# Kernel tuning notes

Measured on AMD Instinct MI355X. Metric: run time of the kernel, lower is better.

## Reference

```python
import jax, jax.numpy as jnp
import numpy as np
import math

B, S, HID = 1, 4096, 2048
NH, NKV, DH = 8, 1, 256
ROPE_BASE = 10000.0


def setup_inputs() -> dict:
    key = jax.random.key(0)
    ks = jax.random.split(key, 5)
    sc = 0.02
    return {
        "hidden_states": jax.random.normal(ks[0], (B, S, HID), dtype=jnp.float32),
        "position_ids": jnp.arange(S, dtype=jnp.int32)[None, :].repeat(B, axis=0),
        "wq": jax.random.normal(ks[1], (HID, NH * DH), dtype=jnp.float32) * sc,
        "wk": jax.random.normal(ks[2], (HID, NKV * DH), dtype=jnp.float32) * sc,
        "wv": jax.random.normal(ks[3], (HID, NKV * DH), dtype=jnp.float32) * sc,
        "wo": jax.random.normal(ks[4], (NH * DH, HID), dtype=jnp.float32) * sc,
    }


def _rope_cos_sin(position_ids, dtype):
    # inv_freq: [DH/2]
    inv_freq = 1.0 / (ROPE_BASE ** (jnp.arange(0, DH, 2, dtype=jnp.float32) / DH))
    # freqs: [B, S, DH/2]
    freqs = position_ids.astype(jnp.float32)[:, :, None] * inv_freq[None, None, :]
    emb = jnp.concatenate([freqs, freqs], axis=-1)  # [B, S, DH]
    return jnp.cos(emb).astype(dtype), jnp.sin(emb).astype(dtype)


def _rotate_half(x):
    x1, x2 = x[..., : DH // 2], x[..., DH // 2 :]
    return jnp.concatenate([-x2, x1], axis=-1)


def reference(hidden_states, position_ids, wq, wk, wv, wo):
    bsz, q_len, _ = hidden_states.shape
    dtype = hidden_states.dtype

    # QKV projections (bias=False)
    q = (hidden_states @ wq).reshape(bsz, q_len, NH, DH).transpose(0, 2, 1, 3)   # [B,NH,S,DH]
    k = (hidden_states @ wk).reshape(bsz, q_len, NKV, DH).transpose(0, 2, 1, 3)  # [B,NKV,S,DH]
    v = (hidden_states @ wv).reshape(bsz, q_len, NKV, DH).transpose(0, 2, 1, 3)  # [B,NKV,S,DH]

    # RoPE (unsqueeze_dim=1 -> broadcast over heads)
    cos, sin = _rope_cos_sin(position_ids, dtype)
    cos, sin = cos[:, None, :, :], sin[:, None, :, :]  # [B,1,S,DH]
    q = q * cos + _rotate_half(q) * sin
    k = k * cos + _rotate_half(k) * sin

    # GQA: k/v broadcast over the NH head dim via matmul broadcasting (repeat_kv)
    scores = jnp.matmul(q, jnp.swapaxes(k, -1, -2)) / math.sqrt(DH)  # [B,NH,S,S]

    # additive causal mask (0 on/below diagonal, -inf-ish above)
    neg = jnp.finfo(jnp.float32).min
    causal = jnp.where(
        jnp.tril(jnp.ones((q_len, q_len), dtype=bool)), 0.0, neg
    ).astype(jnp.float32)[None, None, :, :]
    scores = scores + causal

    probs = jax.nn.softmax(scores.astype(jnp.float32), axis=-1).astype(dtype)
    attn = jnp.matmul(probs, v)  # [B,NH,S,DH] (v broadcasts over NH)

    attn = attn.transpose(0, 2, 1, 3).reshape(bsz, q_len, NH * DH)
    return attn @ wo
```

## Files before the change

### kernel.cpp

```cpp
#include <hip/hip_runtime.h>
#include <hip/hip_bf16.h>

typedef __bf16 bf16;
typedef __attribute__((ext_vector_type(8))) __bf16 bf16x8;
typedef __attribute__((ext_vector_type(4))) float f32x4;

#define S_LEN  4096
#define HIDDEN 2048
#define N_HEADS 8
#define D_HEAD 256
#define QKV_N  2560
#define NEG_BIG (-1e30f)
#define MFIX 8.0f

#define OFF_WQKVT 0u
#define OFF_WOT   10485760u
#define OFF_QKV   18874368u
#define OFF_VT    39845888u
#define OFF_AOUT  41943040u
#define OFF_FLAG  58720256u
#define WS_NEED   58720320u
#define OFF_PBUF  0u
#define OFF_LBUF  8388608u

__global__ __launch_bounds__(256) void detect_dtype(const unsigned short* __restrict__ w,
                                                    int* __restrict__ flag) {
  __shared__ int bad;
  if (threadIdx.x == 0) bad = 0;
  __syncthreads();
  int local = 0;
  for (int i = threadIdx.x; i < 4096; i += 256) {
    int e = (w[i] >> 7) & 0xFF;
    if (e >= 130) local = 1;
  }
  if (local) atomicOr(&bad, 1);
  __syncthreads();
  if (threadIdx.x == 0) *flag = bad;
}

__device__ __forceinline__ bf16x8 load8(const void* p, size_t idx, bool f32) {
  if (f32) {
    const float* q = (const float*)p + idx;
    bf16x8 r;
#pragma unroll
    for (int j = 0; j < 8; ++j) r[j] = (bf16)q[j];
    return r;
  }
  return *(const bf16x8*)((const bf16*)p + idx);
}

__global__ __launch_bounds__(256) void cvt_hs(const void* __restrict__ hs,
                                              bf16* __restrict__ dst,
                                              const int* __restrict__ flag) {
  bool f32 = (*flag != 0);
  size_t i = ((size_t)blockIdx.x * 256 + threadIdx.x) * 8;
  *(bf16x8*)(dst + i) = load8(hs, i, f32);
}

__device__ __forceinline__ void transpose_tile64(const void* __restrict__ src, size_t sbase,
                                                 int sld, bool f32,
                                                 bf16* __restrict__ dst, int dld,
                                                 bf16 (*T)[72]) {
  int tid = threadIdx.x;
  int r  = tid >> 2;
  int c4 = (tid & 3) * 16;
  *(bf16x8*)(&T[r][c4])     = load8(src, sbase + (size_t)r * sld + c4, f32);
  *(bf16x8*)(&T[r][c4 + 8]) = load8(src, sbase + (size_t)r * sld + c4 + 8, f32);
  __syncthreads();
  bf16x8 v0, v1;
#pragma unroll
  for (int j = 0; j < 8; ++j) { v0[j] = T[c4 + j][r]; v1[j] = T[c4 + 8 + j][r]; }
  *(bf16x8*)(dst + (size_t)r * dld + c4)     = v0;
  *(bf16x8*)(dst + (size_t)r * dld + c4 + 8) = v1;
}

__global__ __launch_bounds__(256) void build_wqkvT(const void* __restrict__ wq,
                                                   const void* __restrict__ wk,
                                                   const void* __restrict__ wv,
                                                   bf16* __restrict__ dst,
                                                   const int* __restrict__ flag) {
  __shared__ __align__(16) bf16 T[64][72];
  bool f32 = (*flag != 0);
  int n0 = blockIdx.x * 64;
  int k0 = blockIdx.y * 64;
  const void* src; int ld, c0;
  if (n0 < 2048)      { src = wq; ld = 2048; c0 = n0; }
  else if (n0 < 2304) { src = wk; ld = 256;  c0 = n0 - 2048; }
  else                { src = wv; ld = 256;  c0 = n0 - 2304; }
  transpose_tile64(src, (size_t)k0 * ld + c0, ld, f32,
                   dst + (size_t)n0 * HIDDEN + k0, HIDDEN, T);
}

__global__ __launch_bounds__(256) void transpose_any(const void* __restrict__ src, int sbase,
                                                     int sld,
                                                     bf16* __restrict__ dst, int dld,
                                                     const int* __restrict__ flag) {
  __shared__ __align__(16) bf16 T[64][72];
  bool f32 = flag && (*flag != 0);
  int c0 = blockIdx.x * 64;
  int r0 = blockIdx.y * 64;
  transpose_tile64(src, (size_t)sbase + (size_t)r0 * sld + c0, sld, f32,
                   dst + (size_t)c0 * dld + r0, dld, T);
}

__device__ __forceinline__ void gload16(const bf16* g, bf16* l) {
  __builtin_amdgcn_global_load_lds((__attribute__((address_space(1))) void*)(void*)g,
                                   (__attribute__((address_space(3))) void*)(void*)l,
                                   16, 0, 0);
}

__global__ __launch_bounds__(256) void gemm_bk64(const bf16* __restrict__ A,
                                                 const bf16* __restrict__ BT,
                                                 void* __restrict__ C,
                                                 int M, int N, int K,
                                                 const int* __restrict__ cflag) {
  __shared__ __align__(16) bf16 As[2][128 * 64];
  __shared__ __align__(16) bf16 Bs[2][128 * 64];
  bool cf32 = cflag && (*cflag != 0);
  int tid  = threadIdx.x;
  int w = tid >> 6, lane = tid & 63;
  int quad = lane >> 4, l16 = lane & 15;
  int bm = blockIdx.y * 128, bn = blockIdx.x * 128;
  int wm = (w >> 1) * 64, wn = (w & 1) * 64;

  int lr = lane >> 3, lc = lane & 7;
  int scol = ((lc ^ lr) << 3);
  const bf16* Ag[4]; const bf16* Bg[4];
#pragma unroll
  for (int j = 0; j < 4; ++j) {
    int row = (w * 4 + j) * 8 + lr;
    Ag[j] = A  + (size_t)(bm + row) * K + scol;
    Bg[j] = BT + (size_t)(bn + row) * K + scol;
  }

  int nIter = K >> 6;
#pragma unroll
  for (int j = 0; j < 4; ++j) {
    gload16(Ag[j], &As[0][(w * 4 + j) * 512]);
    gload16(Bg[j], &Bs[0][(w * 4 + j) * 512]);
  }
  __syncthreads();

  int cA = ((quad    ) ^ (l16 & 7)) << 3;
  int cB = ((quad + 4) ^ (l16 & 7)) << 3;

  f32x4 acc[4][4] = {};
  for (int kt = 0; kt < nIter; ++kt) {
    int cur = kt & 1;
    if (kt + 1 < nIter) {
      int nxt = cur ^ 1;
      int koff = (kt + 1) << 6;
#pragma unroll
      for (int j = 0; j < 4; ++j) {
        gload16(Ag[j] + koff, &As[nxt][(w * 4 + j) * 512]);
        gload16(Bg[j] + koff, &Bs[nxt][(w * 4 + j) * 512]);
      }
    }
    const bf16* Ab = &As[cur][0];
    const bf16* Bb = &Bs[cur][0];
#pragma unroll
    for (int h = 0; h < 2; ++h) {
      int cc = h ? cB : cA;
      bf16x8 af[4], bfr[4];
#pragma unroll
      for (int mt = 0; mt < 4; ++mt)
        af[mt] = *(const bf16x8*)(Ab + (wm + mt * 16 + l16) * 64 + cc);
#pragma unroll
      for (int nt = 0; nt < 4; ++nt)
        bfr[nt] = *(const bf16x8*)(Bb + (wn + nt * 16 + l16) * 64 + cc);
#pragma unroll
      for (int mt = 0; mt < 4; ++mt)
#pragma unroll
        for (int nt = 0; nt < 4; ++nt)
          acc[mt][nt] = __builtin_amdgcn_mfma_f32_16x16x32_bf16(af[mt], bfr[nt],
                                                                acc[mt][nt], 0, 0, 0);
    }
    __syncthreads();
  }

#pragma unroll
  for (int mt = 0; mt < 4; ++mt)
#pragma unroll
    for (int nt = 0; nt < 4; ++nt)
#pragma unroll
      for (int r = 0; r < 4; ++r) {
        int row = bm + wm + mt * 16 + quad * 4 + r;
        int col = bn + wn + nt * 16 + l16;
        size_t off = (size_t)row * N + col;
        float v = acc[mt][nt][r];
        if (cf32) ((float*)C)[off] = v;
        else      ((bf16*)C)[off] = (bf16)v;
      }
}

__global__ __launch_bounds__(256) void rope_kernel(bf16* __restrict__ qkv,
                                                   const int* __restrict__ pos) {
  int s = blockIdx.x;
  float p = (float)pos[s];
  bf16* row = qkv + (size_t)s * QKV_N;
  for (int i = threadIdx.x; i < 9 * 128; i += 256) {
    int h = i >> 7, d = i & 127;
    float inv = __expf(-(float)d * (9.210340371976184f / 128.0f));
    float th = p * inv;
    float sn, c;
    sincosf(th, &sn, &c);
    c  = (float)(bf16)c;
    sn = (float)(bf16)sn;
    bf16* x = row + ((h < 8) ? h * 256 : 2048);
    float x1 = (float)x[d], x2 = (float)x[d + 128];
    x[d]       = (bf16)(x1 * c - x2 * sn);
    x[d + 128] = (bf16)(x2 * c + x1 * sn);
  }
}

__global__ __launch_bounds__(256, 2) void attn_kernel(const bf16* __restrict__ qkv,
                                                      const bf16* __restrict__ VT,
                                                      bf16* __restrict__ aout,
                                                      bf16* __restrict__ pbuf,
                                                      float* __restrict__ lbuf) {
  __shared__ __align__(16) bf16 Ks[64 * 256];
  __shared__ __align__(16) bf16 Vs[256 * 64];
  __shared__ __align__(16) bf16 Pl[4][16][72];
  int tid  = threadIdx.x;
  int w = tid >> 6, lane = tid & 63;
  int quad = lane >> 4, l16 = lane & 15;
  int b    = blockIdx.x;
  int head = b & 7;
  int t    = b >> 3;
  int a    = t & 31, which = t >> 5;
  int qtBig = 63 - a;

  int nseg, sqt[2], sk0[2], sk1[2], smode[2];
  if (which == 0) {
    nseg = 1; sqt[0] = qtBig; sk0[0] = 0; sk1[0] = 33;
    smode[0] = (a == 31) ? 0 : 1;
  } else if (a == 31) {
    nseg = 1; sqt[0] = 31; sk0[0] = 0; sk1[0] = 32; smode[0] = 0;
  } else {
    nseg = 2;
    sqt[0] = qtBig; sk0[0] = 33; sk1[0] = qtBig + 1; smode[0] = 2;
    sqt[1] = a;     sk0[1] = 0;  sk1[1] = a + 1;     smode[1] = 0;
  }

  int kro = tid >> 5, kcc = tid & 31;
  int vro = tid >> 3, vcc = tid & 7;

  for (int sg = 0; sg < nseg; ++sg) {
    int qt = sqt[sg], k0 = sk0[sg], k1 = sk1[sg], mode = smode[sg];
    int qw = qt * 64 + w * 16;

    const bf16* qrow = qkv + (size_t)(qw + l16) * QKV_N + head * D_HEAD + quad * 8;
    bf16x8 qf[8];
#pragma unroll
    for (int dc = 0; dc < 8; ++dc) {
      bf16x8 tq = *(const bf16x8*)(qrow + dc * 32);
#pragma unroll
      for (int j = 0; j < 8; ++j) tq[j] = (bf16)((float)tq[j] * 0.0625f);
      qf[dc] = tq;
    }

    f32x4 o[16] = {};
    float lsum[4] = {0.f, 0.f, 0.f, 0.f};

    bf16x8 kpre[8], vpre[8];
    int kv0p = k0 << 6;
#pragma unroll
    for (int c = 0; c < 8; ++c) {
      kpre[c] = *(const bf16x8*)(qkv + (size_t)(kv0p + c * 8 + kro) * QKV_N + 2048 + kcc * 8);
      vpre[c] = *(const bf16x8*)(VT + (size_t)(c * 32 + vro) * S_LEN + kv0p + vcc * 8);
    }

    for (int kt = k0; kt < k1; ++kt) {
      __syncthreads();
#pragma unroll
      for (int c = 0; c < 8; ++c) {
        int r  = c * 8 + kro;
        *(bf16x8*)(Ks + r * 256 + ((kcc ^ (r & 31)) * 8)) = kpre[c];
        int rv = c * 32 + vro;
        *(bf16x8*)(Vs + rv * 64 + ((vcc ^ (rv & 7)) * 8)) = vpre[c];
      }
      __syncthreads();
      if (kt + 1 < k1) {
        int kv1 = (kt + 1) << 6;
#pragma unroll
        for (int c = 0; c < 8; ++c) {
          kpre[c] = *(const bf16x8*)(qkv + (size_t)(kv1 + c * 8 + kro) * QKV_N + 2048 + kcc * 8);
          vpre[c] = *(const bf16x8*)(VT + (size_t)(c * 32 + vro) * S_LEN + kv1 + vcc * 8);
        }
      }
      f32x4 sv[4] = {};
      __builtin_amdgcn_s_setprio(1);
#pragma unroll
      for (int dc = 0; dc < 8; ++dc)
#pragma unroll
        for (int n = 0; n < 4; ++n) {
          int row = n * 16 + l16;
          bf16x8 kf = *(const bf16x8*)(Ks + row * 256 + (((dc << 2) + quad) ^ (row & 31)) * 8);
          sv[n] = __builtin_amdgcn_mfma_f32_16x16x32_bf16(qf[dc], kf, sv[n], 0, 0, 0);
        }
      __builtin_amdgcn_s_setprio(0);
      bool diag = (kt == qt);
      float pv4[4][4];
#pragma unroll
      for (int n = 0; n < 4; ++n)
#pragma unroll
        for (int r = 0; r < 4; ++r) {
          float x = sv[n][r] - MFIX;
          if (diag && (n * 16 + l16 > w * 16 + quad * 4 + r)) x = NEG_BIG;
          float e = __expf(x);
          pv4[n][r] = e;
          lsum[r] += e;
        }
#pragma unroll
      for (int n = 0; n < 4; ++n)
#pragma unroll
        for (int r = 0; r < 4; ++r)
          Pl[w][quad * 4 + r][n * 16 + l16] = (bf16)pv4[n][r];
      asm volatile("s_waitcnt lgkmcnt(0)" ::: "memory");
      bf16x8 pa0 = *(const bf16x8*)(&Pl[w][l16][quad * 8]);
      bf16x8 pa1 = *(const bf16x8*)(&Pl[w][l16][32 + quad * 8]);
      __builtin_amdgcn_s_setprio(1);
#pragma unroll
      for (int dt = 0; dt < 16; ++dt) {
        int row = dt * 16 + l16;
        const bf16* vb = Vs + row * 64;
        bf16x8 v0 = *(const bf16x8*)(vb + ((quad)     ^ (row & 7)) * 8);
        bf16x8 v1 = *(const bf16x8*)(vb + ((4 + quad) ^ (row & 7)) * 8);
        o[dt] = __builtin_amdgcn_mfma_f32_16x16x32_bf16(pa0, v0, o[dt], 0, 0, 0);
        o[dt] = __builtin_amdgcn_mfma_f32_16x16x32_bf16(pa1, v1, o[dt], 0, 0, 0);
      }
      __builtin_amdgcn_s_setprio(0);
    }

    float lrow[4];
#pragma unroll
    for (int r = 0; r < 4; ++r) lrow[r] = lsum[r];
#pragma unroll
    for (int off = 8; off >= 1; off >>= 1)
#pragma unroll
      for (int r = 0; r < 4; ++r)
        lrow[r] += __shfl_xor(lrow[r], off, 16);

    if (mode == 0) {
      float invl[4];
#pragma unroll
      for (int r = 0; r < 4; ++r) invl[r] = 1.0f / lrow[r];
      bf16* orow = aout + (size_t)(qw + quad * 4) * HIDDEN + head * D_HEAD + l16;
#pragma unroll
      for (int dt = 0; dt < 16; ++dt)
#pragma unroll
        for (int r = 0; r < 4; ++r)
          orow[(size_t)r * HIDDEN + dt * 16] = (bf16)(o[dt][r] * invl[r]);
    } else {
      if (mode == 1) {
        bf16* orow = aout + (size_t)(qw + quad * 4) * HIDDEN + head * D_HEAD + l16;
#pragma unroll
        for (int dt = 0; dt < 16; ++dt)
#pragma unroll
          for (int r = 0; r < 4; ++r)
            orow[(size_t)r * HIDDEN + dt * 16] = (bf16)o[dt][r];
      } else {
        int pidx = head * 31 + a;
        bf16* orow = pbuf + ((size_t)pidx * 64 + w * 16 + quad * 4) * 256 + l16;
#pragma unroll
        for (int dt = 0; dt < 16; ++dt)
#pragma unroll
          for (int r = 0; r < 4; ++r)
            orow[(size_t)r * 256 + dt * 16] = (bf16)o[dt][r];
      }
      if (l16 == 0) {
        int pidx = head * 31 + a;
        int base = (pidx * 2 + which) * 64 + w * 16 + quad * 4;
#pragma unroll
        for (int r = 0; r < 4; ++r) lbuf[base + r] = lrow[r];
      }
    }
  }
}

__global__ __launch_bounds__(256) void combine_kernel(bf16* __restrict__ aout,
                                                      const bf16* __restrict__ pbuf,
                                                      const float* __restrict__ lbuf) {
  int p = blockIdx.x;
  int h = p / 31, a = p % 31;
  int qtBig = 63 - a;
  int tid = threadIdx.x;
  for (int i = tid; i < 2048; i += 256) {
    int rowin = i >> 5;
    int d8 = (i & 31) * 8;
    int row = qtBig * 64 + rowin;
    float l = lbuf[(p * 2 + 0) * 64 + rowin] + lbuf[(p * 2 + 1) * 64 + rowin];
    float inv = 1.0f / l;
    bf16* ap = aout + (size_t)row * HIDDEN + h * D_HEAD + d8;
    const bf16* bp = pbuf + ((size_t)p * 64 + rowin) * 256 + d8;
    bf16x8 va = *(const bf16x8*)ap;
    bf16x8 vb = *(const bf16x8*)bp;
    bf16x8 vo;
#pragma unroll
    for (int j = 0; j < 8; ++j)
      vo[j] = (bf16)(((float)va[j] + (float)vb[j]) * inv);
    *(bf16x8*)ap = vo;
  }
}

extern "C" void kernel_launch(void* const* d_in, const int* in_sizes, int n_in,
                              void* d_out, int out_size, void* d_ws, size_t ws_size,
                              hipStream_t stream) {
  if (ws_size < (size_t)WS_NEED) return;
  const void* hs  = d_in[0];
  const int*  pos = (const int*)d_in[1];
  const void* wq  = d_in[2];
  const void* wk  = d_in[3];
  const void* wv  = d_in[4];
  const void* wo  = d_in[5];

  char* ws = (char*)d_ws;
  bf16* wqkvT = (bf16*)(ws + OFF_WQKVT);
  bf16* woT   = (bf16*)(ws + OFF_WOT);
  bf16* qkv   = (bf16*)(ws + OFF_QKV);
  bf16* VT    = (bf16*)(ws + OFF_VT);
  bf16* aout  = (bf16*)(ws + OFF_AOUT);
  int*  flag  = (int*)(ws + OFF_FLAG);
  bf16*  pbuf = (bf16*)(ws + OFF_PBUF);
  float* lbuf = (float*)(ws + OFF_LBUF);
  bf16*  hsb  = aout;

  detect_dtype<<<1, 256, 0, stream>>>((const unsigned short*)wq, flag);
  build_wqkvT<<<dim3(QKV_N / 64, HIDDEN / 64), 256, 0, stream>>>(wq, wk, wv, wqkvT, flag);
  transpose_any<<<dim3(HIDDEN / 64, HIDDEN / 64), 256, 0, stream>>>(wo, 0, HIDDEN,
                                                                    woT, HIDDEN, flag);
  cvt_hs<<<(S_LEN * HIDDEN) / (256 * 8), 256, 0, stream>>>(hs, hsb, flag);
  gemm_bk64<<<dim3(QKV_N / 128, S_LEN / 128), 256, 0, stream>>>(hsb, wqkvT, qkv,
                                                                S_LEN, QKV_N, HIDDEN,
                                                                nullptr);
  rope_kernel<<<S_LEN, 256, 0, stream>>>(qkv, pos);
  transpose_any<<<dim3(D_HEAD / 64, S_LEN / 64), 256, 0, stream>>>(qkv, 2304, QKV_N,
                                                                   VT, S_LEN, nullptr);
  attn_kernel<<<N_HEADS * 64, 256, 0, stream>>>(qkv, VT, aout, pbuf, lbuf);
  combine_kernel<<<248, 256, 0, stream>>>(aout, pbuf, lbuf);
  gemm_bk64<<<dim3(HIDDEN / 128, S_LEN / 128), 256, 0, stream>>>(aout, woT, d_out,
                                                                 S_LEN, HIDDEN, HIDDEN,
                                                                 flag);
}
```

Baseline: 355.4 us.

## Double-buffer attention K/V via async LDS loads, use 128-row query tiles, swizzle GEMM blocks

The attention kernel now uses 512-thread blocks covering 128 query rows, which halves the block count and reuses each K/V tile across more queries. K/V tiles are double-buffered in LDS with global_load_lds, replacing register staging, so the next tile's load overlaps the current tile's compute. The causal split and the combine kernel are reworked for 128-row tiles. The GEMM also remaps block IDs with a stride-8 swizzle to improve L2 locality. LDS use doubles to about 160KB per block, which may limit occupancy, and the launch grid shrinks to 256 blocks.

```diff
diff --git a/kernel.cpp b/kernel.cpp
--- a/kernel.cpp
+++ b/kernel.cpp
@@ -120,7 +120,12 @@
   int tid  = threadIdx.x;
   int w = tid >> 6, lane = tid & 63;
   int quad = lane >> 4, l16 = lane & 15;
-  int bm = blockIdx.y * 128, bn = blockIdx.x * 128;
+
+  int nx = gridDim.x;
+  int nwg = nx * gridDim.y;
+  int bid = blockIdx.y * nx + blockIdx.x;
+  int swz = (bid & 7) * (nwg >> 3) + (bid >> 3);
+  int bm = (swz / nx) * 128, bn = (swz % nx) * 128;
   int wm = (w >> 1) * 64, wn = (w & 1) * 64;
 
   int lr = lane >> 3, lc = lane & 7;
@@ -213,43 +218,55 @@
   }
 }
 
-__global__ __launch_bounds__(256, 2) void attn_kernel(const bf16* __restrict__ qkv,
+__device__ __forceinline__ void stage_kv(const bf16* __restrict__ qkv,
+                                         const bf16* __restrict__ VT,
+                                         bf16* __restrict__ kb, bf16* __restrict__ vb,
+                                         int kv0, int w, int lane) {
+#pragma unroll
+  for (int i = 0; i < 4; ++i) {
+    int seg = w * 4 + i;
+    int rK = seg * 2 + (lane >> 5);
+    int sK = (lane & 31) ^ (rK & 31);
+    gload16(qkv + (size_t)(kv0 + rK) * QKV_N + 2048 + sK * 8, kb + seg * 512);
+    int rV = seg * 8 + (lane >> 3);
+    int sV = (lane & 7) ^ (rV & 7);
+    gload16(VT + (size_t)rV * S_LEN + kv0 + sV * 8, vb + seg * 512);
+  }
+}
+
+__global__ __launch_bounds__(512, 2) void attn_kernel(const bf16* __restrict__ qkv,
                                                       const bf16* __restrict__ VT,
                                                       bf16* __restrict__ aout,
                                                       bf16* __restrict__ pbuf,
                                                       float* __restrict__ lbuf) {
-  __shared__ __align__(16) bf16 Ks[64 * 256];
-  __shared__ __align__(16) bf16 Vs[256 * 64];
-  __shared__ __align__(16) bf16 Pl[4][16][72];
+  __shared__ __align__(16) bf16 Ks[2][64 * 256];
+  __shared__ __align__(16) bf16 Vs[2][256 * 64];
+  __shared__ __align__(16) bf16 Pl[8][16][72];
   int tid  = threadIdx.x;
   int w = tid >> 6, lane = tid & 63;
   int quad = lane >> 4, l16 = lane & 15;
-  int b    = blockIdx.x;
-  int head = b & 7;
-  int t    = b >> 3;
-  int a    = t & 31, which = t >> 5;
-  int qtBig = 63 - a;
+  int bx   = blockIdx.x;
+  int head = bx & 7;
+  int t    = bx >> 3;
+  int a    = t & 15, which = t >> 4;
+  int qBig = 31 - a;
+  int tilesBig = 2 * qBig + 2;
 
   int nseg, sqt[2], sk0[2], sk1[2], smode[2];
   if (which == 0) {
-    nseg = 1; sqt[0] = qtBig; sk0[0] = 0; sk1[0] = 33;
-    smode[0] = (a == 31) ? 0 : 1;
-  } else if (a == 31) {
-    nseg = 1; sqt[0] = 31; sk0[0] = 0; sk1[0] = 32; smode[0] = 0;
+    nseg = 1; sqt[0] = qBig; sk0[0] = 0;  sk1[0] = 33;        smode[0] = 1;
   } else {
     nseg = 2;
-    sqt[0] = qtBig; sk0[0] = 33; sk1[0] = qtBig + 1; smode[0] = 2;
-    sqt[1] = a;     sk0[1] = 0;  sk1[1] = a + 1;     smode[1] = 0;
-  }
-
-  int kro = tid >> 5, kcc = tid & 31;
-  int vro = tid >> 3, vcc = tid & 7;
+    sqt[0] = qBig; sk0[0] = 33; sk1[0] = tilesBig;  smode[0] = 2;
+    sqt[1] = a;    sk0[1] = 0;  sk1[1] = 2 * a + 2; smode[1] = 0;
+  }
+  int pidx = head * 16 + a;
 
   for (int sg = 0; sg < nseg; ++sg) {
     int qt = sqt[sg], k0 = sk0[sg], k1 = sk1[sg], mode = smode[sg];
-    int qw = qt * 64 + w * 16;
-
-    const bf16* qrow = qkv + (size_t)(qw + l16) * QKV_N + head * D_HEAD + quad * 8;
+    int qrow_w = qt * 128 + w * 16;
+
+    const bf16* qrow = qkv + (size_t)(qrow_w + l16) * QKV_N + head * D_HEAD + quad * 8;
     bf16x8 qf[8];
 #pragma unroll
     for (int dc = 0; dc < 8; ++dc) {
@@ -262,32 +279,15 @@
     f32x4 o[16] = {};
     float lsum[4] = {0.f, 0.f, 0.f, 0.f};
 
-    bf16x8 kpre[8], vpre[8];
-    int kv0p = k0 << 6;
-#pragma unroll
-    for (int c = 0; c < 8; ++c) {
-      kpre[c] = *(const bf16x8*)(qkv + (size_t)(kv0p + c * 8 + kro) * QKV_N + 2048 + kcc * 8);
-      vpre[c] = *(const bf16x8*)(VT + (size_t)(c * 32 + vro) * S_LEN + kv0p + vcc * 8);
-    }
+    __syncthreads();
+    stage_kv(qkv, VT, Ks[0], Vs[0], k0 << 6, w, lane);
 
     for (int kt = k0; kt < k1; ++kt) {
+      int par = (kt - k0) & 1;
       __syncthreads();
-#pragma unroll
-      for (int c = 0; c < 8; ++c) {
-        int r  = c * 8 + kro;
-        *(bf16x8*)(Ks + r * 256 + ((kcc ^ (r & 31)) * 8)) = kpre[c];
-        int rv = c * 32 + vro;
-        *(bf16x8*)(Vs + rv * 64 + ((vcc ^ (rv & 7)) * 8)) = vpre[c];
-      }
-      __syncthreads();
-      if (kt + 1 < k1) {
-        int kv1 = (kt + 1) << 6;
-#pragma unroll
-        for (int c = 0; c < 8; ++c) {
-          kpre[c] = *(const bf16x8*)(qkv + (size_t)(kv1 + c * 8 + kro) * QKV_N + 2048 + kcc * 8);
-          vpre[c] = *(const bf16x8*)(VT + (size_t)(c * 32 + vro) * S_LEN + kv1 + vcc * 8);
-        }
-      }
+      if (kt + 1 < k1)
+        stage_kv(qkv, VT, Ks[par ^ 1], Vs[par ^ 1], (kt + 1) << 6, w, lane);
+
       f32x4 sv[4] = {};
       __builtin_amdgcn_s_setprio(1);
 #pragma unroll
@@ -295,18 +295,20 @@
 #pragma unroll
         for (int n = 0; n < 4; ++n) {
           int row = n * 16 + l16;
-          bf16x8 kf = *(const bf16x8*)(Ks + row * 256 + (((dc << 2) + quad) ^ (row & 31)) * 8);
+          bf16x8 kf = *(const bf16x8*)(Ks[par] + row * 256 +
+                                       (((dc << 2) + quad) ^ (row & 31)) * 8);
           sv[n] = __builtin_amdgcn_mfma_f32_16x16x32_bf16(qf[dc], kf, sv[n], 0, 0, 0);
         }
       __builtin_amdgcn_s_setprio(0);
-      bool diag = (kt == qt);
+
+      bool dg = (kt * 64 + 63) > qrow_w;
       float pv4[4][4];
 #pragma unroll
       for (int n = 0; n < 4; ++n)
 #pragma unroll
         for (int r = 0; r < 4; ++r) {
           float x = sv[n][r] - MFIX;
-          if (diag && (n * 16 + l16 > w * 16 + quad * 4 + r)) x = NEG_BIG;
+          if (dg && (kt * 64 + n * 16 + l16 > qrow_w + quad * 4 + r)) x = NEG_BIG;
           float e = __expf(x);
           pv4[n][r] = e;
           lsum[r] += e;
@@ -319,13 +321,14 @@
       asm volatile("s_waitcnt lgkmcnt(0)" ::: "memory");
       bf16x8 pa0 = *(const bf16x8*)(&Pl[w][l16][quad * 8]);
       bf16x8 pa1 = *(const bf16x8*)(&Pl[w][l16][32 + quad * 8]);
+
       __builtin_amdgcn_s_setprio(1);
 #pragma unroll
       for (int dt = 0; dt < 16; ++dt) {
         int row = dt * 16 + l16;
-        const bf16* vb = Vs + row * 64;
-        bf16x8 v0 = *(const bf16x8*)(vb + ((quad)     ^ (row & 7)) * 8);
-        bf16x8 v1 = *(const bf16x8*)(vb + ((4 + quad) ^ (row & 7)) * 8);
+        const bf16* vb2 = Vs[par] + row * 64;
+        bf16x8 v0 = *(const bf16x8*)(vb2 + ((quad)     ^ (row & 7)) * 8);
+        bf16x8 v1 = *(const bf16x8*)(vb2 + ((4 + quad) ^ (row & 7)) * 8);
         o[dt] = __builtin_amdgcn_mfma_f32_16x16x32_bf16(pa0, v0, o[dt], 0, 0, 0);
         o[dt] = __builtin_amdgcn_mfma_f32_16x16x32_bf16(pa1, v1, o[dt], 0, 0, 0);
       }
@@ -340,12 +343,13 @@
 #pragma unroll
       for (int r = 0; r < 4; ++r)
         lrow[r] += __shfl_xor(lrow[r], off, 16);
+    int rowb = w * 16 + quad * 4;
 
     if (mode == 0) {
       float invl[4];
 #pragma unroll
       for (int r = 0; r < 4; ++r) invl[r] = 1.0f / lrow[r];
-      bf16* orow = aout + (size_t)(qw + quad * 4) * HIDDEN + head * D_HEAD + l16;
+      bf16* orow = aout + (size_t)(qt * 128 + rowb) * HIDDEN + head * D_HEAD + l16;
 #pragma unroll
       for (int dt = 0; dt < 16; ++dt)
 #pragma unroll
@@ -353,15 +357,14 @@
           orow[(size_t)r * HIDDEN + dt * 16] = (bf16)(o[dt][r] * invl[r]);
     } else {
       if (mode == 1) {
-        bf16* orow = aout + (size_t)(qw + quad * 4) * HIDDEN + head * D_HEAD + l16;
+        bf16* orow = aout + (size_t)(qt * 128 + rowb) * HIDDEN + head * D_HEAD + l16;
 #pragma unroll
         for (int dt = 0; dt < 16; ++dt)
 #pragma unroll
           for (int r = 0; r < 4; ++r)
             orow[(size_t)r * HIDDEN + dt * 16] = (bf16)o[dt][r];
       } else {
-        int pidx = head * 31 + a;
-        bf16* orow = pbuf + ((size_t)pidx * 64 + w * 16 + quad * 4) * 256 + l16;
+        bf16* orow = pbuf + ((size_t)pidx * 128 + rowb) * 256 + l16;
 #pragma unroll
         for (int dt = 0; dt < 16; ++dt)
 #pragma unroll
@@ -369,8 +372,7 @@
             orow[(size_t)r * 256 + dt * 16] = (bf16)o[dt][r];
       }
       if (l16 == 0) {
-        int pidx = head * 31 + a;
-        int base = (pidx * 2 + which) * 64 + w * 16 + quad * 4;
+        int base = (pidx * 2 + which) * 128 + rowb;
 #pragma unroll
         for (int r = 0; r < 4; ++r) lbuf[base + r] = lrow[r];
       }
@@ -382,17 +384,16 @@
                                                       const bf16* __restrict__ pbuf,
                                                       const float* __restrict__ lbuf) {
   int p = blockIdx.x;
-  int h = p / 31, a = p % 31;
-  int qtBig = 63 - a;
+  int h = p >> 4, a = p & 15;
+  int qBig = 31 - a;
   int tid = threadIdx.x;
-  for (int i = tid; i < 2048; i += 256) {
+  for (int i = tid; i < 4096; i += 256) {
     int rowin = i >> 5;
     int d8 = (i & 31) * 8;
-    int row = qtBig * 64 + rowin;
-    float l = lbuf[(p * 2 + 0) * 64 + rowin] + lbuf[(p * 2 + 1) * 64 + rowin];
+    float l = lbuf[(p * 2 + 0) * 128 + rowin] + lbuf[(p * 2 + 1) * 128 + rowin];
     float inv = 1.0f / l;
-    bf16* ap = aout + (size_t)row * HIDDEN + h * D_HEAD + d8;
-    const bf16* bp = pbuf + ((size_t)p * 64 + rowin) * 256 + d8;
+    bf16* ap = aout + (size_t)(qBig * 128 + rowin) * HIDDEN + h * D_HEAD + d8;
+    const bf16* bp = pbuf + ((size_t)p * 128 + rowin) * 256 + d8;
     bf16x8 va = *(const bf16x8*)ap;
     bf16x8 vb = *(const bf16x8*)bp;
     bf16x8 vo;
@@ -436,8 +437,8 @@
   rope_kernel<<<S_LEN, 256, 0, stream>>>(qkv, pos);
   transpose_any<<<dim3(D_HEAD / 64, S_LEN / 64), 256, 0, stream>>>(qkv, 2304, QKV_N,
                                                                    VT, S_LEN, nullptr);
-  attn_kernel<<<N_HEADS * 64, 256, 0, stream>>>(qkv, VT, aout, pbuf, lbuf);
-  combine_kernel<<<248, 256, 0, stream>>>(aout, pbuf, lbuf);
+  attn_kernel<<<N_HEADS * 32, 512, 0, stream>>>(qkv, VT, aout, pbuf, lbuf);
+  combine_kernel<<<128, 256, 0, stream>>>(aout, pbuf, lbuf);
   gemm_bk64<<<dim3(HIDDEN / 128, S_LEN / 128), 256, 0, stream>>>(aout, woT, d_out,
                                                                  S_LEN, HIDDEN, HIDDEN,
                                                                  flag);
```

Result: no change. 353.8 us (-0.5%).

## Stage attention K/V via direct global-to-LDS loads and swizzle GEMM block order

Applied to the files above, without the earlier changes.

Replaces the register-prefetched K/V tiles in the attention kernel with direct global_load_lds transfers into swizzled shared memory. This frees the prefetch registers, but the load is now issued synchronously each iteration with no double buffering, so latency is no longer overlapped with compute. The GEMM also remaps block IDs with an 8-way interleave, aiming at better L2 locality. The diagonal mask test is rewritten in absolute row and column coordinates.

```diff
diff --git a/kernel.cpp b/kernel.cpp
--- a/kernel.cpp
+++ b/kernel.cpp
@@ -120,7 +120,12 @@
   int tid  = threadIdx.x;
   int w = tid >> 6, lane = tid & 63;
   int quad = lane >> 4, l16 = lane & 15;
-  int bm = blockIdx.y * 128, bn = blockIdx.x * 128;
+
+  int nx = gridDim.x;
+  int nwg = nx * gridDim.y;
+  int bid = blockIdx.y * nx + blockIdx.x;
+  int swz = (bid & 7) * (nwg >> 3) + (bid >> 3);
+  int bm = (swz / nx) * 128, bn = (swz % nx) * 128;
   int wm = (w >> 1) * 64, wn = (w & 1) * 64;
 
   int lr = lane >> 3, lc = lane & 7;
@@ -213,6 +218,22 @@
   }
 }
 
+__device__ __forceinline__ void stage_kv(const bf16* __restrict__ qkv,
+                                         const bf16* __restrict__ VT,
+                                         bf16* __restrict__ kb, bf16* __restrict__ vb,
+                                         int kv0, int w, int lane) {
+#pragma unroll
+  for (int i = 0; i < 8; ++i) {
+    int seg = w * 8 + i;
+    int rK = seg * 2 + (lane >> 5);
+    int sK = (lane & 31) ^ (rK & 31);
+    gload16(qkv + (size_t)(kv0 + rK) * QKV_N + 2048 + sK * 8, kb + seg * 512);
+    int rV = seg * 8 + (lane >> 3);
+    int sV = (lane & 7) ^ (rV & 7);
+    gload16(VT + (size_t)rV * S_LEN + kv0 + sV * 8, vb + seg * 512);
+  }
+}
+
 __global__ __launch_bounds__(256, 2) void attn_kernel(const bf16* __restrict__ qkv,
                                                       const bf16* __restrict__ VT,
                                                       bf16* __restrict__ aout,
@@ -241,15 +262,13 @@
     sqt[0] = qtBig; sk0[0] = 33; sk1[0] = qtBig + 1; smode[0] = 2;
     sqt[1] = a;     sk0[1] = 0;  sk1[1] = a + 1;     smode[1] = 0;
   }
-
-  int kro = tid >> 5, kcc = tid & 31;
-  int vro = tid >> 3, vcc = tid & 7;
+  int pidx = head * 31 + a;
 
   for (int sg = 0; sg < nseg; ++sg) {
     int qt = sqt[sg], k0 = sk0[sg], k1 = sk1[sg], mode = smode[sg];
-    int qw = qt * 64 + w * 16;
-
-    const bf16* qrow = qkv + (size_t)(qw + l16) * QKV_N + head * D_HEAD + quad * 8;
+    int qrow_w = qt * 64 + w * 16;
+
+    const bf16* qrow = qkv + (size_t)(qrow_w + l16) * QKV_N + head * D_HEAD + quad * 8;
     bf16x8 qf[8];
 #pragma unroll
     for (int dc = 0; dc < 8; ++dc) {
@@ -262,32 +281,12 @@
     f32x4 o[16] = {};
     float lsum[4] = {0.f, 0.f, 0.f, 0.f};
 
-    bf16x8 kpre[8], vpre[8];
-    int kv0p = k0 << 6;
-#pragma unroll
-    for (int c = 0; c < 8; ++c) {
-      kpre[c] = *(const bf16x8*)(qkv + (size_t)(kv0p + c * 8 + kro) * QKV_N + 2048 + kcc * 8);
-      vpre[c] = *(const bf16x8*)(VT + (size_t)(c * 32 + vro) * S_LEN + kv0p + vcc * 8);
-    }
-
     for (int kt = k0; kt < k1; ++kt) {
+      int kv0 = kt << 6;
       __syncthreads();
-#pragma unroll
-      for (int c = 0; c < 8; ++c) {
-        int r  = c * 8 + kro;
-        *(bf16x8*)(Ks + r * 256 + ((kcc ^ (r & 31)) * 8)) = kpre[c];
-        int rv = c * 32 + vro;
-        *(bf16x8*)(Vs + rv * 64 + ((vcc ^ (rv & 7)) * 8)) = vpre[c];
-      }
+      stage_kv(qkv, VT, Ks, Vs, kv0, w, lane);
       __syncthreads();
-      if (kt + 1 < k1) {
-        int kv1 = (kt + 1) << 6;
-#pragma unroll
-        for (int c = 0; c < 8; ++c) {
-          kpre[c] = *(const bf16x8*)(qkv + (size_t)(kv1 + c * 8 + kro) * QKV_N + 2048 + kcc * 8);
-          vpre[c] = *(const bf16x8*)(VT + (size_t)(c * 32 + vro) * S_LEN + kv1 + vcc * 8);
-        }
-      }
+
       f32x4 sv[4] = {};
       __builtin_amdgcn_s_setprio(1);
 #pragma unroll
@@ -295,18 +294,20 @@
 #pragma unroll
         for (int n = 0; n < 4; ++n) {
           int row = n * 16 + l16;
-          bf16x8 kf = *(const bf16x8*)(Ks + row * 256 + (((dc << 2) + quad) ^ (row & 31)) * 8);
+          bf16x8 kf = *(const bf16x8*)(Ks + row * 256 +
+                                       (((dc << 2) + quad) ^ (row & 31)) * 8);
           sv[n] = __builtin_amdgcn_mfma_f32_16x16x32_bf16(qf[dc], kf, sv[n], 0, 0, 0);
         }
       __builtin_amdgcn_s_setprio(0);
-      bool diag = (kt == qt);
+
+      bool dg = (kv0 + 63) > qrow_w;
       float pv4[4][4];
 #pragma unroll
       for (int n = 0; n < 4; ++n)
 #pragma unroll
         for (int r = 0; r < 4; ++r) {
           float x = sv[n][r] - MFIX;
-          if (diag && (n * 16 + l16 > w * 16 + quad * 4 + r)) x = NEG_BIG;
+          if (dg && (kv0 + n * 16 + l16 > qrow_w + quad * 4 + r)) x = NEG_BIG;
           float e = __expf(x);
           pv4[n][r] = e;
           lsum[r] += e;
@@ -319,13 +320,14 @@
       asm volatile("s_waitcnt lgkmcnt(0)" ::: "memory");
       bf16x8 pa0 = *(const bf16x8*)(&Pl[w][l16][quad * 8]);
       bf16x8 pa1 = *(const bf16x8*)(&Pl[w][l16][32 + quad * 8]);
+
       __builtin_amdgcn_s_setprio(1);
 #pragma unroll
       for (int dt = 0; dt < 16; ++dt) {
         int row = dt * 16 + l16;
-        const bf16* vb = Vs + row * 64;
-        bf16x8 v0 = *(const bf16x8*)(vb + ((quad)     ^ (row & 7)) * 8);
-        bf16x8 v1 = *(const bf16x8*)(vb + ((4 + quad) ^ (row & 7)) * 8);
+        const bf16* vb2 = Vs + row * 64;
+        bf16x8 v0 = *(const bf16x8*)(vb2 + ((quad)     ^ (row & 7)) * 8);
+        bf16x8 v1 = *(const bf16x8*)(vb2 + ((4 + quad) ^ (row & 7)) * 8);
         o[dt] = __builtin_amdgcn_mfma_f32_16x16x32_bf16(pa0, v0, o[dt], 0, 0, 0);
         o[dt] = __builtin_amdgcn_mfma_f32_16x16x32_bf16(pa1, v1, o[dt], 0, 0, 0);
       }
@@ -345,7 +347,7 @@
       float invl[4];
 #pragma unroll
       for (int r = 0; r < 4; ++r) invl[r] = 1.0f / lrow[r];
-      bf16* orow = aout + (size_t)(qw + quad * 4) * HIDDEN + head * D_HEAD + l16;
+      bf16* orow = aout + (size_t)(qrow_w + quad * 4) * HIDDEN + head * D_HEAD + l16;
 #pragma unroll
       for (int dt = 0; dt < 16; ++dt)
 #pragma unroll
@@ -353,14 +355,13 @@
           orow[(size_t)r * HIDDEN + dt * 16] = (bf16)(o[dt][r] * invl[r]);
     } else {
       if (mode == 1) {
-        bf16* orow = aout + (size_t)(qw + quad * 4) * HIDDEN + head * D_HEAD + l16;
+        bf16* orow = aout + (size_t)(qrow_w + quad * 4) * HIDDEN + head * D_HEAD + l16;
 #pragma unroll
         for (int dt = 0; dt < 16; ++dt)
 #pragma unroll
           for (int r = 0; r < 4; ++r)
             orow[(size_t)r * HIDDEN + dt * 16] = (bf16)o[dt][r];
       } else {
-        int pidx = head * 31 + a;
         bf16* orow = pbuf + ((size_t)pidx * 64 + w * 16 + quad * 4) * 256 + l16;
 #pragma unroll
         for (int dt = 0; dt < 16; ++dt)
@@ -369,7 +370,6 @@
             orow[(size_t)r * 256 + dt * 16] = (bf16)o[dt][r];
       }
       if (l16 == 0) {
-        int pidx = head * 31 + a;
         int base = (pidx * 2 + which) * 64 + w * 16 + quad * 4;
 #pragma unroll
         for (int r = 0; r < 4; ++r) lbuf[base + r] = lrow[r];
```

After: 346.0 us. 1.03x faster.
